# Performance work log

Hardware: AMD Instinct MI355X
Metric: run time of the kernel (lower is better)

The kernel has to match this reference:

```python
import jax, jax.numpy as jnp
import numpy as np

N_NODES = 100_000
N_EDGES = 3_200_000  # avg in-degree 32
N_CLASSES = 16
TEMP = 0.5


def setup_inputs() -> dict:
    key = jax.random.key(0)
    k1, k2, k3 = jax.random.split(key, 3)
    src = jax.random.randint(k1, (N_EDGES,), 0, N_NODES, dtype=jnp.int32)
    # guarantee every node has at least one incoming edge so scatter-mean
    # and the sharpening normalization are well-defined
    dst = jnp.concatenate([
        jnp.arange(N_NODES, dtype=jnp.int32),
        jax.random.randint(k2, (N_EDGES - N_NODES,), 0, N_NODES, dtype=jnp.int32),
    ])
    edge_index = jnp.stack([src, dst], axis=0)  # [2, E]
    # positive predictions (log is taken downstream)
    aug_pred = jax.random.uniform(k3, (N_NODES, N_CLASSES), jnp.float32, 1e-3, 1.0)
    return {"edge_index": edge_index, "aug_pred": aug_pred}


def reference(edge_index, aug_pred):
    src = edge_index[0]  # message source nodes
    dst = edge_index[1]  # aggregation targets
    E = edge_index.shape[1]

    # scatter-mean aggregation: avg_pred[i] = mean_{e: dst[e]=i} aug_pred[src[e]]
    msg = aug_pred[src]                                   # [E, C]
    sums = jax.ops.segment_sum(msg, dst, num_segments=N_NODES)
    cnt = jax.ops.segment_sum(jnp.ones((E,), aug_pred.dtype), dst,
                              num_segments=N_NODES)
    avg_pred = sums / jnp.maximum(cnt, 1.0)[:, None]      # [N, C]

    # temperature sharpening + normalize
    p = avg_pred ** (1.0 / TEMP)
    sharp_avg_pred = p / jnp.sum(p, axis=1, keepdims=True)

    # edge-indexed gathers; dst side is detached in the original
    s = (avg_pred + 1e-10)[src]                            # [E, C]
    d = jax.lax.stop_gradient(sharp_avg_pred + 1e-10)[dst]  # [E, C]

    cr_loss = (d * jnp.log(d) - d * jnp.log(s)).sum(axis=1)  # [E]
    return cr_loss.mean()
```

## Files before the change

kernel.cpp:

```cpp
#include <hip/hip_runtime.h>

#define NCLS 16
#define NB 391
#define BSH 8
#define TILE 8192
#define BTHR 512
#define KPT 16
#define CAP 10240
#define ACAP 10
#define ASTR 17

static __device__ __forceinline__ float bflo(unsigned u) {
  return __uint_as_float(u << 16);
}
static __device__ __forceinline__ float bfhi(unsigned u) {
  return __uint_as_float(u & 0xFFFF0000u);
}
static __device__ __forceinline__ unsigned f2bf1(float f) {
  unsigned u = __float_as_uint(f);
  return (u + 0x7FFF + ((u >> 16) & 1)) >> 16;
}
static __device__ __forceinline__ unsigned packbf(float a, float b) {
  return f2bf1(a) | (f2bf1(b) << 16);
}

__global__ void __launch_bounds__(BTHR) bin_kernel(const int* __restrict__ srcv,
                                                   const int* __restrict__ dstv,
                                                   const float2* __restrict__ aug,
                                                   unsigned* __restrict__ augh,
                                                   int* __restrict__ gcur,
                                                   int* __restrict__ packed,
                                                   int E, int n2) {
  __shared__ int hist[NB];
  __shared__ int off[NB];
  __shared__ int delta[NB];
  __shared__ int part[16];
  __shared__ int2 stag[TILE];
  int tid = threadIdx.x;
  for (int i = blockIdx.x * BTHR + tid; i < n2; i += gridDim.x * BTHR) {
    float2 v = aug[i];
    augh[i] = packbf(v.x, v.y);
  }
  int base = blockIdx.x * TILE;
  int cnt = min(TILE, E - base);
  for (int t = tid; t < NB; t += BTHR) hist[t] = 0;
  __syncthreads();
  int myw[KPT];
  int myp[KPT];
#pragma unroll
  for (int k = 0; k < KPT; k++) {
    int idx = tid + k * BTHR;
    myw[k] = -1;
    myp[k] = 0;
    if (idx < cnt) {
      int s = srcv[base + idx], d = dstv[base + idx];
      int b = d >> BSH;
      int r = atomicAdd(&hist[b], 1);
      myw[k] = s | ((d & 255) << 17);
      myp[k] = (b << 13) | r;
    }
  }
  __syncthreads();
  if (tid < 16) {
    int s = 0;
    int lo = tid * 25, hiX = min(NB, lo + 25);
    for (int j = lo; j < hiX; j++) { int v = hist[j]; off[j] = s; s += v; }
    part[tid] = s;
  }
  __syncthreads();
  if (tid == 0) {
    int run = 0;
    for (int j = 0; j < 16; j++) { int v = part[j]; part[j] = run; run += v; }
  }
  __syncthreads();
  for (int t = tid; t < NB; t += BTHR) off[t] += part[t / 25];
  __syncthreads();
  for (int t = tid; t < NB; t += BTHR) {
    int c = hist[t];
    int gb = c ? atomicAdd(&gcur[t], c) : 0;
    delta[t] = t * CAP + gb - off[t];
  }
  __syncthreads();
#pragma unroll
  for (int k = 0; k < KPT; k++) {
    if (myw[k] >= 0) {
      int b = myp[k] >> 13, r = myp[k] & 8191;
      int p = off[b] + r;
      int2 w;
      w.x = myw[k];
      w.y = p + delta[b];
      stag[p] = w;
    }
  }
  __syncthreads();
  for (int i = tid; i < cnt; i += BTHR) {
    int2 w = stag[i];
    packed[w.y] = w.x;
  }
}

__global__ void __launch_bounds__(1024) agg_kernel(const int* __restrict__ gcur,
                                                   const int* __restrict__ packed,
                                                   const unsigned* __restrict__ augh,
                                                   unsigned* __restrict__ logs,
                                                   unsigned* __restrict__ dvech,
                                                   double* __restrict__ acc, int N) {
  __shared__ int ssrc[CAP];
  __shared__ int hist[256];
  __shared__ int off[256];
  __shared__ float red[16];
  int tid = threadIdx.x;
  int b = blockIdx.x;
  int rbeg = b * CAP;
  int cnt = gcur[b];
  if (tid < 256) hist[tid] = 0;
  __syncthreads();
  int myw[ACAP];
  int myr[ACAP];
#pragma unroll
  for (int k = 0; k < ACAP; k++) {
    int i = tid + k * 1024;
    int w = (i < cnt) ? packed[rbeg + i] : -1;
    myw[k] = w;
    myr[k] = (w >= 0) ? atomicAdd(&hist[w >> 17], 1) : 0;
  }
  __syncthreads();
  if (tid < 64) {
    int h0 = hist[4 * tid], h1 = hist[4 * tid + 1];
    int h2 = hist[4 * tid + 2], h3 = hist[4 * tid + 3];
    int tot = h0 + h1 + h2 + h3;
    int inc = tot;
#pragma unroll
    for (int o = 1; o < 64; o <<= 1) {
      int u = __shfl_up(inc, o, 64);
      if (tid >= o) inc += u;
    }
    int exc = inc - tot;
    off[4 * tid] = exc;
    off[4 * tid + 1] = exc + h0;
    off[4 * tid + 2] = exc + h0 + h1;
    off[4 * tid + 3] = exc + h0 + h1 + h2;
  }
  __syncthreads();
#pragma unroll
  for (int k = 0; k < ACAP; k++) {
    int w = myw[k];
    if (w >= 0) ssrc[off[w >> 17] + myr[k]] = w & 0x1FFFF;
  }
  __syncthreads();
  int node = tid >> 2, lane = tid & 3;
  int par = lane & 1, half = lane >> 1;
  int boff = off[node];
  int deg = hist[node];
  int woff = half << 2;
  double s0 = 0., s1 = 0., s2 = 0., s3 = 0., s4 = 0., s5 = 0., s6 = 0., s7 = 0.;
  int e = par;
  for (; e + 6 < deg; e += 8) {
    int q0 = ssrc[boff + e],     q1 = ssrc[boff + e + 2];
    int q2 = ssrc[boff + e + 4], q3 = ssrc[boff + e + 6];
    uint4 g0 = *reinterpret_cast<const uint4*>(augh + ((size_t)q0 << 3) + woff);
    uint4 g1 = *reinterpret_cast<const uint4*>(augh + ((size_t)q1 << 3) + woff);
    uint4 g2 = *reinterpret_cast<const uint4*>(augh + ((size_t)q2 << 3) + woff);
    uint4 g3 = *reinterpret_cast<const uint4*>(augh + ((size_t)q3 << 3) + woff);
    s0 += (double)bflo(g0.x) + (double)bflo(g1.x) + (double)bflo(g2.x) + (double)bflo(g3.x);
    s1 += (double)bfhi(g0.x) + (double)bfhi(g1.x) + (double)bfhi(g2.x) + (double)bfhi(g3.x);
    s2 += (double)bflo(g0.y) + (double)bflo(g1.y) + (double)bflo(g2.y) + (double)bflo(g3.y);
    s3 += (double)bfhi(g0.y) + (double)bfhi(g1.y) + (double)bfhi(g2.y) + (double)bfhi(g3.y);
    s4 += (double)bflo(g0.z) + (double)bflo(g1.z) + (double)bflo(g2.z) + (double)bflo(g3.z);
    s5 += (double)bfhi(g0.z) + (double)bfhi(g1.z) + (double)bfhi(g2.z) + (double)bfhi(g3.z);
    s6 += (double)bflo(g0.w) + (double)bflo(g1.w) + (double)bflo(g2.w) + (double)bflo(g3.w);
    s7 += (double)bfhi(g0.w) + (double)bfhi(g1.w) + (double)bfhi(g2.w) + (double)bfhi(g3.w);
  }
  for (; e < deg; e += 2) {
    int q0 = ssrc[boff + e];
    uint4 g0 = *reinterpret_cast<const uint4*>(augh + ((size_t)q0 << 3) + woff);
    s0 += (double)bflo(g0.x); s1 += (double)bfhi(g0.x);
    s2 += (double)bflo(g0.y); s3 += (double)bfhi(g0.y);
    s4 += (double)bflo(g0.z); s5 += (double)bfhi(g0.z);
    s6 += (double)bflo(g0.w); s7 += (double)bfhi(g0.w);
  }
  s0 += __shfl_xor(s0, 1, 64); s1 += __shfl_xor(s1, 1, 64);
  s2 += __shfl_xor(s2, 1, 64); s3 += __shfl_xor(s3, 1, 64);
  s4 += __shfl_xor(s4, 1, 64); s5 += __shfl_xor(s5, 1, 64);
  s6 += __shfl_xor(s6, 1, 64); s7 += __shfl_xor(s7, 1, 64);
  double dinv = 1.0 / (double)(deg > 0 ? deg : 1);
  float a0 = (float)(s0 * dinv), a1 = (float)(s1 * dinv);
  float a2 = (float)(s2 * dinv), a3 = (float)(s3 * dinv);
  float a4 = (float)(s4 * dinv), a5 = (float)(s5 * dinv);
  float a6 = (float)(s6 * dinv), a7 = (float)(s7 * dinv);
  float p2 = a0 * a0 + a1 * a1 + a2 * a2 + a3 * a3 +
             a4 * a4 + a5 * a5 + a6 * a6 + a7 * a7;
  p2 += __shfl_xor(p2, 2, 64);
  float ip = 1.0f / p2;
  float d0 = a0 * a0 * ip + 1e-10f, d1 = a1 * a1 * ip + 1e-10f;
  float d2 = a2 * a2 * ip + 1e-10f, d3 = a3 * a3 * ip + 1e-10f;
  float d4 = a4 * a4 * ip + 1e-10f, d5 = a5 * a5 * ip + 1e-10f;
  float d6 = a6 * a6 * ip + 1e-10f, d7 = a7 * a7 * ip + 1e-10f;
  float h = d0 * __logf(d0) + d1 * __logf(d1) + d2 * __logf(d2) + d3 * __logf(d3) +
            d4 * __logf(d4) + d5 * __logf(d5) + d6 * __logf(d6) + d7 * __logf(d7);
  h += __shfl_xor(h, 2, 64);
  int g = (b << BSH) + node;
  float contrib = 0.f;
  if (g < N) {
    if (par == 0) {
      uint4 lw;
      lw.x = packbf(__logf(a0 + 1e-10f), __logf(a1 + 1e-10f));
      lw.y = packbf(__logf(a2 + 1e-10f), __logf(a3 + 1e-10f));
      lw.z = packbf(__logf(a4 + 1e-10f), __logf(a5 + 1e-10f));
      lw.w = packbf(__logf(a6 + 1e-10f), __logf(a7 + 1e-10f));
      *reinterpret_cast<uint4*>(logs + ((size_t)g << 3) + woff) = lw;
      uint2 dw;
      dw.x = packbf(d0, d1);
      dw.y = packbf(d2, d3);
      uint2 dw2;
      dw2.x = packbf(d4, d5);
      dw2.y = packbf(d6, d7);
      uint4 dq;
      dq.x = dw.x; dq.y = dw.y; dq.z = dw2.x; dq.w = dw2.y;
      *reinterpret_cast<uint4*>(dvech + ((size_t)g << 3) + woff) = dq;
    }
    if (lane == 0) contrib = (float)deg * (h + __shfl_xor(h, 0, 64) * 0.f);
    if (lane == 0) contrib = (float)deg * h;
  }
#pragma unroll
  for (int o = 32; o >= 1; o >>= 1) contrib += __shfl_xor(contrib, o, 64);
  if ((tid & 63) == 0) red[tid >> 6] = contrib;
  __syncthreads();
  if (tid == 0) {
    float s = 0.f;
#pragma unroll
    for (int wv = 0; wv < 16; wv++) s += red[wv];
    atomicAdd(acc, (double)s);
  }
}

__global__ void __launch_bounds__(1024) loss_kernel(const int* __restrict__ gcur,
                                                    const int* __restrict__ packed,
                                                    const unsigned* __restrict__ logs,
                                                    const unsigned* __restrict__ dvech,
                                                    double* __restrict__ acc,
                                                    int* __restrict__ done,
                                                    float* __restrict__ out,
                                                    int N, int E) {
  __shared__ float sdv[256 * ASTR];
  __shared__ double red[16];
  int tid = threadIdx.x;
  int b = blockIdx.x;
  int rbeg = b * CAP;
  int cnt = gcur[b];
  int rend = rbeg + cnt;
  int nb0 = b << BSH;
  {
    const uint2* gsrc = reinterpret_cast<const uint2*>(dvech + ((size_t)nb0 << 3));
    int nvalid = min(256, N - nb0);
    int nq = nvalid * 4;
    for (int i = tid; i < nq; i += 1024) {
      uint2 v = gsrc[i];
      float* r = sdv + (i >> 2) * ASTR + ((i & 3) << 2);
      r[0] = bflo(v.x); r[1] = bfhi(v.x);
      r[2] = bflo(v.y); r[3] = bfhi(v.y);
    }
  }
  __syncthreads();
  double dot = 0.0;
  int i = rbeg + tid;
  for (; i + 1024 < rend; i += 2048) {
    int wa = packed[i];
    int wb = packed[i + 1024];
    int sa = wa & 0x1FFFF, la = wa >> 17;
    int sb = wb & 0x1FFFF, lb = wb >> 17;
    const uint4* ga = reinterpret_cast<const uint4*>(logs + ((size_t)sa << 3));
    const uint4* gb = reinterpret_cast<const uint4*>(logs + ((size_t)sb << 3));
    uint4 a0 = ga[0], a1 = ga[1];
    uint4 b0 = gb[0], b1 = gb[1];
    const float* ra = sdv + la * ASTR;
    const float* rb = sdv + lb * ASTR;
    float ea = ra[0] * bflo(a0.x) + ra[1] * bfhi(a0.x) +
               ra[2] * bflo(a0.y) + ra[3] * bfhi(a0.y) +
               ra[4] * bflo(a0.z) + ra[5] * bfhi(a0.z) +
               ra[6] * bflo(a0.w) + ra[7] * bfhi(a0.w) +
               ra[8] * bflo(a1.x) + ra[9] * bfhi(a1.x) +
               ra[10] * bflo(a1.y) + ra[11] * bfhi(a1.y) +
               ra[12] * bflo(a1.z) + ra[13] * bfhi(a1.z) +
               ra[14] * bflo(a1.w) + ra[15] * bfhi(a1.w);
    float eb = rb[0] * bflo(b0.x) + rb[1] * bfhi(b0.x) +
               rb[2] * bflo(b0.y) + rb[3] * bfhi(b0.y) +
               rb[4] * bflo(b0.z) + rb[5] * bfhi(b0.z) +
               rb[6] * bflo(b0.w) + rb[7] * bfhi(b0.w) +
               rb[8] * bflo(b1.x) + rb[9] * bfhi(b1.x) +
               rb[10] * bflo(b1.y) + rb[11] * bfhi(b1.y) +
               rb[12] * bflo(b1.z) + rb[13] * bfhi(b1.z) +
               rb[14] * bflo(b1.w) + rb[15] * bfhi(b1.w);
    dot += (double)ea + (double)eb;
  }
  if (i < rend) {
    int wa = packed[i];
    int sa = wa & 0x1FFFF, la = wa >> 17;
    const uint4* ga = reinterpret_cast<const uint4*>(logs + ((size_t)sa << 3));
    uint4 a0 = ga[0], a1 = ga[1];
    const float* ra = sdv + la * ASTR;
    float ea = ra[0] * bflo(a0.x) + ra[1] * bfhi(a0.x) +
               ra[2] * bflo(a0.y) + ra[3] * bfhi(a0.y) +
               ra[4] * bflo(a0.z) + ra[5] * bfhi(a0.z) +
               ra[6] * bflo(a0.w) + ra[7] * bfhi(a0.w) +
               ra[8] * bflo(a1.x) + ra[9] * bfhi(a1.x) +
               ra[10] * bflo(a1.y) + ra[11] * bfhi(a1.y) +
               ra[12] * bflo(a1.z) + ra[13] * bfhi(a1.z) +
               ra[14] * bflo(a1.w) + ra[15] * bfhi(a1.w);
    dot += (double)ea;
  }
#pragma unroll
  for (int o = 32; o >= 1; o >>= 1) dot += __shfl_xor(dot, o, 64);
  if ((tid & 63) == 0) red[tid >> 6] = dot;
  __syncthreads();
  if (tid == 0) {
    double s = 0.0;
#pragma unroll
    for (int wv = 0; wv < 16; wv++) s += red[wv];
    atomicAdd(acc, -s);
    __threadfence();
    int t = atomicAdd(done, 1);
    if (t == (int)gridDim.x - 1) {
      double v = atomicAdd(acc, 0.0);
      out[0] = (float)(v / (double)E);
    }
  }
}

extern "C" void kernel_launch(void* const* d_in, const int* in_sizes, int n_in,
                              void* d_out, int out_size, void* d_ws, size_t ws_size,
                              hipStream_t stream) {
  const int* edge_index = (const int*)d_in[0];
  const float* aug_pred = (const float*)d_in[1];
  const int E = in_sizes[0] / 2;
  const int N = in_sizes[1] / NCLS;

  const int* srcv = edge_index;
  const int* dstv = edge_index + E;

  char* p = (char*)d_ws;
  auto alloc = [&](size_t bytes) {
    char* r = p;
    p += (bytes + 255) & ~(size_t)255;
    return r;
  };
  double* acc = (double*)alloc(8);
  int* done = (int*)alloc(4);
  int* gcur = (int*)alloc(NB * 4);
  int* packed = (int*)alloc((size_t)NB * CAP * 4);
  unsigned* augh = (unsigned*)alloc((size_t)N * NCLS * 2);
  unsigned* logs = (unsigned*)alloc((size_t)N * NCLS * 2);
  unsigned* dvech = (unsigned*)alloc((size_t)N * NCLS * 2);

  size_t zero_bytes = (size_t)((char*)packed - (char*)d_ws);
  hipMemsetAsync(d_ws, 0, zero_bytes, stream);

  int n2 = N * NCLS / 2;
  int tiles = (E + TILE - 1) / TILE;
  bin_kernel<<<tiles, BTHR, 0, stream>>>(srcv, dstv, (const float2*)aug_pred,
                                         augh, gcur, packed, E, n2);
  agg_kernel<<<NB, 1024, 0, stream>>>(gcur, packed, augh, logs, dvech, acc, N);
  loss_kernel<<<NB, 1024, 0, stream>>>(gcur, packed, logs, dvech, acc, done,
                                       (float*)d_out, N, E);
}
```

Before: 149.7 us.

## Read loss edges directly from edge_index with grid-stride instead of binned LDS tiles

The loss kernel no longer walks the dst-binned packed edge list and stages each bin's dvec rows in shared memory. It now grid-strides over the original src/dst arrays and gathers both the log row and the sharpened-target row from global memory for every edge. This removes the shared-memory staging and the per-bin load imbalance and gives a fully occupied, evenly split grid. In exchange it adds a random 32-byte global gather per edge for dvech plus reads of two index arrays, where before it read one packed index.

```diff
diff --git a/kernel.cpp b/kernel.cpp
--- a/kernel.cpp
+++ b/kernel.cpp
@@ -8,7 +8,6 @@
 #define KPT 16
 #define CAP 10240
 #define ACAP 10
-#define ASTR 17
 
 static __device__ __forceinline__ float bflo(unsigned u) {
   return __uint_as_float(u << 16);
@@ -209,17 +208,13 @@
       lw.z = packbf(__logf(a4 + 1e-10f), __logf(a5 + 1e-10f));
       lw.w = packbf(__logf(a6 + 1e-10f), __logf(a7 + 1e-10f));
       *reinterpret_cast<uint4*>(logs + ((size_t)g << 3) + woff) = lw;
-      uint2 dw;
-      dw.x = packbf(d0, d1);
-      dw.y = packbf(d2, d3);
-      uint2 dw2;
-      dw2.x = packbf(d4, d5);
-      dw2.y = packbf(d6, d7);
       uint4 dq;
-      dq.x = dw.x; dq.y = dw.y; dq.z = dw2.x; dq.w = dw2.y;
+      dq.x = packbf(d0, d1);
+      dq.y = packbf(d2, d3);
+      dq.z = packbf(d4, d5);
+      dq.w = packbf(d6, d7);
       *reinterpret_cast<uint4*>(dvech + ((size_t)g << 3) + woff) = dq;
     }
-    if (lane == 0) contrib = (float)deg * (h + __shfl_xor(h, 0, 64) * 0.f);
     if (lane == 0) contrib = (float)deg * h;
   }
 #pragma unroll
@@ -234,79 +229,62 @@
   }
 }
 
-__global__ void __launch_bounds__(1024) loss_kernel(const int* __restrict__ gcur,
-                                                    const int* __restrict__ packed,
-                                                    const unsigned* __restrict__ logs,
-                                                    const unsigned* __restrict__ dvech,
-                                                    double* __restrict__ acc,
-                                                    int* __restrict__ done,
-                                                    float* __restrict__ out,
-                                                    int N, int E) {
-  __shared__ float sdv[256 * ASTR];
-  __shared__ double red[16];
+__global__ void __launch_bounds__(256) loss_kernel(const int* __restrict__ srcv,
+                                                   const int* __restrict__ dstv,
+                                                   const unsigned* __restrict__ logs,
+                                                   const unsigned* __restrict__ dvech,
+                                                   double* __restrict__ acc,
+                                                   int* __restrict__ done,
+                                                   float* __restrict__ out, int E) {
+  __shared__ double red[4];
   int tid = threadIdx.x;
-  int b = blockIdx.x;
-  int rbeg = b * CAP;
-  int cnt = gcur[b];
-  int rend = rbeg + cnt;
-  int nb0 = b << BSH;
-  {
-    const uint2* gsrc = reinterpret_cast<const uint2*>(dvech + ((size_t)nb0 << 3));
-    int nvalid = min(256, N - nb0);
-    int nq = nvalid * 4;
-    for (int i = tid; i < nq; i += 1024) {
-      uint2 v = gsrc[i];
-      float* r = sdv + (i >> 2) * ASTR + ((i & 3) << 2);
-      r[0] = bflo(v.x); r[1] = bfhi(v.x);
-      r[2] = bflo(v.y); r[3] = bfhi(v.y);
-    }
-  }
-  __syncthreads();
+  int i0 = blockIdx.x * 256 + tid;
+  int stride = gridDim.x * 256;
   double dot = 0.0;
-  int i = rbeg + tid;
-  for (; i + 1024 < rend; i += 2048) {
-    int wa = packed[i];
-    int wb = packed[i + 1024];
-    int sa = wa & 0x1FFFF, la = wa >> 17;
-    int sb = wb & 0x1FFFF, lb = wb >> 17;
-    const uint4* ga = reinterpret_cast<const uint4*>(logs + ((size_t)sa << 3));
-    const uint4* gb = reinterpret_cast<const uint4*>(logs + ((size_t)sb << 3));
-    uint4 a0 = ga[0], a1 = ga[1];
-    uint4 b0 = gb[0], b1 = gb[1];
-    const float* ra = sdv + la * ASTR;
-    const float* rb = sdv + lb * ASTR;
-    float ea = ra[0] * bflo(a0.x) + ra[1] * bfhi(a0.x) +
-               ra[2] * bflo(a0.y) + ra[3] * bfhi(a0.y) +
-               ra[4] * bflo(a0.z) + ra[5] * bfhi(a0.z) +
-               ra[6] * bflo(a0.w) + ra[7] * bfhi(a0.w) +
-               ra[8] * bflo(a1.x) + ra[9] * bfhi(a1.x) +
-               ra[10] * bflo(a1.y) + ra[11] * bfhi(a1.y) +
-               ra[12] * bflo(a1.z) + ra[13] * bfhi(a1.z) +
-               ra[14] * bflo(a1.w) + ra[15] * bfhi(a1.w);
-    float eb = rb[0] * bflo(b0.x) + rb[1] * bfhi(b0.x) +
-               rb[2] * bflo(b0.y) + rb[3] * bfhi(b0.y) +
-               rb[4] * bflo(b0.z) + rb[5] * bfhi(b0.z) +
-               rb[6] * bflo(b0.w) + rb[7] * bfhi(b0.w) +
-               rb[8] * bflo(b1.x) + rb[9] * bfhi(b1.x) +
-               rb[10] * bflo(b1.y) + rb[11] * bfhi(b1.y) +
-               rb[12] * bflo(b1.z) + rb[13] * bfhi(b1.z) +
-               rb[14] * bflo(b1.w) + rb[15] * bfhi(b1.w);
+  int i = i0;
+  for (; i + stride < E; i += 2 * stride) {
+    int sa = srcv[i], da = dstv[i];
+    int sb = srcv[i + stride], db = dstv[i + stride];
+    const uint4* la = reinterpret_cast<const uint4*>(logs + ((size_t)sa << 3));
+    const uint4* va = reinterpret_cast<const uint4*>(dvech + ((size_t)da << 3));
+    const uint4* lb = reinterpret_cast<const uint4*>(logs + ((size_t)sb << 3));
+    const uint4* vb = reinterpret_cast<const uint4*>(dvech + ((size_t)db << 3));
+    uint4 a0 = la[0], a1 = la[1];
+    uint4 x0 = va[0], x1 = va[1];
+    uint4 b0 = lb[0], b1 = lb[1];
+    uint4 y0 = vb[0], y1 = vb[1];
+    float ea = bflo(x0.x) * bflo(a0.x) + bfhi(x0.x) * bfhi(a0.x) +
+               bflo(x0.y) * bflo(a0.y) + bfhi(x0.y) * bfhi(a0.y) +
+               bflo(x0.z) * bflo(a0.z) + bfhi(x0.z) * bfhi(a0.z) +
+               bflo(x0.w) * bflo(a0.w) + bfhi(x0.w) * bfhi(a0.w) +
+               bflo(x1.x) * bflo(a1.x) + bfhi(x1.x) * bfhi(a1.x) +
+               bflo(x1.y) * bflo(a1.y) + bfhi(x1.y) * bfhi(a1.y) +
+               bflo(x1.z) * bflo(a1.z) + bfhi(x1.z) * bfhi(a1.z) +
+               bflo(x1.w) * bflo(a1.w) + bfhi(x1.w) * bfhi(a1.w);
+    float eb = bflo(y0.x) * bflo(b0.x) + bfhi(y0.x) * bfhi(b0.x) +
+               bflo(y0.y) * bflo(b0.y) + bfhi(y0.y) * bfhi(b0.y) +
+               bflo(y0.z) * bflo(b0.z) + bfhi(y0.z) * bfhi(b0.z) +
+               bflo(y0.w) * bflo(b0.w) + bfhi(y0.w) * bfhi(b0.w) +
+               bflo(y1.x) * bflo(b1.x) + bfhi(y1.x) * bfhi(b1.x) +
+               bflo(y1.y) * bflo(b1.y) + bfhi(y1.y) * bfhi(b1.y) +
+               bflo(y1.z) * bflo(b1.z) + bfhi(y1.z) * bfhi(b1.z) +
+               bflo(y1.w) * bflo(b1.w) + bfhi(y1.w) * bfhi(b1.w);
     dot += (double)ea + (double)eb;
   }
-  if (i < rend) {
-    int wa = packed[i];
-    int sa = wa & 0x1FFFF, la = wa >> 17;
-    const uint4* ga = reinterpret_cast<const uint4*>(logs + ((size_t)sa << 3));
-    uint4 a0 = ga[0], a1 = ga[1];
-    const float* ra = sdv + la * ASTR;
-    float ea = ra[0] * bflo(a0.x) + ra[1] * bfhi(a0.x) +
-               ra[2] * bflo(a0.y) + ra[3] * bfhi(a0.y) +
-               ra[4] * bflo(a0.z) + ra[5] * bfhi(a0.z) +
-               ra[6] * bflo(a0.w) + ra[7] * bfhi(a0.w) +
-               ra[8] * bflo(a1.x) + ra[9] * bfhi(a1.x) +
-               ra[10] * bflo(a1.y) + ra[11] * bfhi(a1.y) +
-               ra[12] * bflo(a1.z) + ra[13] * bfhi(a1.z) +
-               ra[14] * bflo(a1.w) + ra[15] * bfhi(a1.w);
+  if (i < E) {
+    int sa = srcv[i], da = dstv[i];
+    const uint4* la = reinterpret_cast<const uint4*>(logs + ((size_t)sa << 3));
+    const uint4* va = reinterpret_cast<const uint4*>(dvech + ((size_t)da << 3));
+    uint4 a0 = la[0], a1 = la[1];
+    uint4 x0 = va[0], x1 = va[1];
+    float ea = bflo(x0.x) * bflo(a0.x) + bfhi(x0.x) * bfhi(a0.x) +
+               bflo(x0.y) * bflo(a0.y) + bfhi(x0.y) * bfhi(a0.y) +
+               bflo(x0.z) * bflo(a0.z) + bfhi(x0.z) * bfhi(a0.z) +
+               bflo(x0.w) * bflo(a0.w) + bfhi(x0.w) * bfhi(a0.w) +
+               bflo(x1.x) * bflo(a1.x) + bfhi(x1.x) * bfhi(a1.x) +
+               bflo(x1.y) * bflo(a1.y) + bfhi(x1.y) * bfhi(a1.y) +
+               bflo(x1.z) * bflo(a1.z) + bfhi(x1.z) * bfhi(a1.z) +
+               bflo(x1.w) * bflo(a1.w) + bfhi(x1.w) * bfhi(a1.w);
     dot += (double)ea;
   }
 #pragma unroll
@@ -314,9 +292,7 @@
   if ((tid & 63) == 0) red[tid >> 6] = dot;
   __syncthreads();
   if (tid == 0) {
-    double s = 0.0;
-#pragma unroll
-    for (int wv = 0; wv < 16; wv++) s += red[wv];
+    double s = red[0] + red[1] + red[2] + red[3];
     atomicAdd(acc, -s);
     __threadfence();
     int t = atomicAdd(done, 1);
@@ -360,6 +336,6 @@
   bin_kernel<<<tiles, BTHR, 0, stream>>>(srcv, dstv, (const float2*)aug_pred,
                                          augh, gcur, packed, E, n2);
   agg_kernel<<<NB, 1024, 0, stream>>>(gcur, packed, augh, logs, dvech, acc, N);
-  loss_kernel<<<NB, 1024, 0, stream>>>(gcur, packed, logs, dvech, acc, done,
-                                       (float*)d_out, N, E);
-}
+  loss_kernel<<<2048, 256, 0, stream>>>(srcv, dstv, logs, dvech, acc, done,
+                                        (float*)d_out, E);
+}
```

Measured after the change: 245.8 us. 64.2% more time.
